# Optimization experiments

Hardware: AMD Instinct MI355X
Metric: run time of the kernel (lower is better)

The kernel has to match this reference:

```python
import jax, jax.numpy as jnp
import numpy as np

N, SPLIT, INPUT_DIM = 16384, 100, 128
NUM_HEADS, PER_DIM = 4, 64  # out_dim = 256
NEG_SLOPE = 0.2


def setup_inputs() -> dict:
    key = jax.random.key(0)
    kx, kw, kq = jax.random.split(key, 3)
    x = jax.random.normal(kx, (N, SPLIT * INPUT_DIM), dtype=jnp.float32)
    # glorot-uniform per-head projection weights [H, input_dim, per_dim]
    limit_w = float(np.sqrt(6.0 / (INPUT_DIM + PER_DIM)))
    W = jax.random.uniform(kw, (NUM_HEADS, INPUT_DIM, PER_DIM), dtype=jnp.float32,
                           minval=-limit_w, maxval=limit_w)
    # xavier-uniform query vectors (gain=1.414) for q_ of shape [per_dim, 1] -> stored [H, per_dim]
    limit_q = float(1.414 * np.sqrt(6.0 / (PER_DIM + 1)))
    q = jax.random.uniform(kq, (NUM_HEADS, PER_DIM), dtype=jnp.float32,
                           minval=-limit_q, maxval=limit_q)
    return {"x": x, "W": W, "q": q}


def reference(x, W, q):
    n = x.shape[0]
    xs = x.reshape(n, SPLIT, INPUT_DIM)                      # [n, s, i]
    h = jnp.einsum('nsi,hio->nhso', xs, W)                   # per-head projections
    score = jax.nn.leaky_relu(jnp.einsum('nhso,ho->nhs', h, q), NEG_SLOPE)
    att = jax.nn.softmax(score, axis=2)                      # softmax over split dim
    pooled = jnp.einsum('nhso,nhs->nho', h, att)             # weighted sum pooling
    return pooled.reshape(n, NUM_HEADS * PER_DIM)            # concat heads -> [n, out_dim]
```

## Files before the change

kernel.cpp:

```cpp
#include <hip/hip_runtime.h>
#include <stdint.h>

#define NROWS 16384
#define SPLITN 100
#define IDIM 128
#define NH 4
#define PD 64
#define ROWLEN (SPLITN * IDIM)
#define ODIM (NH * PD)

typedef float f32x4 __attribute__((ext_vector_type(4)));
typedef short s16x8 __attribute__((ext_vector_type(8)));
typedef unsigned short u16x8 __attribute__((ext_vector_type(8)));

__device__ __forceinline__ unsigned short f32_to_bf16(float f) {
  uint32_t u = __float_as_uint(f);
  u += 0x7FFFu + ((u >> 16) & 1u);
  return (unsigned short)(u >> 16);
}

#if __has_builtin(__builtin_amdgcn_exp2f)
__device__ __forceinline__ float fexp2(float x) { return __builtin_amdgcn_exp2f(x); }
#else
__device__ __forceinline__ float fexp2(float x) { return exp2f(x); }
#endif

template <int IMM>
__device__ __forceinline__ float swz_f(float v) {
  return __int_as_float(__builtin_amdgcn_ds_swizzle(__float_as_int(v), IMM));
}

__global__ void prep_wq(const float* __restrict__ W, const float* __restrict__ q,
                        float* __restrict__ wq) {
  int item = blockIdx.x * 256 + threadIdx.x;
  if (item >= NH * IDIM) return;
  int h = item >> 7, i = item & (IDIM - 1);
  const float* wrow = W + (size_t)(h * IDIM + i) * PD;
  const float* qh = q + h * PD;
  float s = 0.f;
#pragma unroll 8
  for (int o = 0; o < PD; ++o) s = __builtin_fmaf(wrow[o], qh[o], s);
  wq[item] = s;
}

__global__ void prep_wp(const float* __restrict__ W, unsigned short* __restrict__ Wp) {
  int flat = blockIdx.x * 256 + threadIdx.x;
  if (flat >= 64 * 512) return;
  int f = flat >> 9;
  int rem = flat & 511;
  int l = rem >> 3, j = rem & 7;
  int of = f & 3, kb = (f >> 2) & 3, h = f >> 4;
  int k = kb * 32 + (l >> 4) * 8 + j;
  int o = of * 16 + (l & 15);
  Wp[flat] = f32_to_bf16(W[(size_t)(h * IDIM + k) * PD + o]);
}

__global__ __launch_bounds__(256) void k1(const float* __restrict__ x,
                                          const float* __restrict__ wq,
                                          unsigned short* __restrict__ ybf) {
  const int lane = threadIdx.x & 63;
  const int g = lane >> 4;
  const int li = lane & 15;
  const int row = (blockIdx.x << 2) | (threadIdx.x >> 6);
  const float* xrow = x + (size_t)row * ROWLEN;

  float wqr[NH][8];
#pragma unroll
  for (int h = 0; h < NH; ++h) {
    f32x4 a = *(const f32x4*)(wq + h * IDIM + li * 8);
    f32x4 b = *(const f32x4*)(wq + h * IDIM + li * 8 + 4);
#pragma unroll
    for (int j = 0; j < 4; ++j) { wqr[h][j] = a[j]; wqr[h][4 + j] = b[j]; }
  }

  float y[NH][8];
  float m[NH], lsum[NH], mL[NH];
#pragma unroll
  for (int h = 0; h < NH; ++h) {
    m[h] = -INFINITY; mL[h] = -INFINITY; lsum[h] = 0.f;
#pragma unroll
    for (int j = 0; j < 8; ++j) y[h][j] = 0.f;
  }
  const float L2E = 1.44269504088896340736f;

  const float* pc = xrow + g * IDIM + li * 8;
  f32x4 xa = *(const f32x4*)pc;
  f32x4 xb = *(const f32x4*)(pc + 4);

  for (int it = 0; it < 25; ++it) {
    f32x4 na = {}, nb = {};
    const float* pn = pc + 4 * IDIM;
    if (it < 24) { na = *(const f32x4*)pn; nb = *(const f32x4*)(pn + 4); }

    float xv[8];
#pragma unroll
    for (int j = 0; j < 4; ++j) { xv[j] = xa[j]; xv[4 + j] = xb[j]; }

    float part[NH];
#pragma unroll
    for (int h = 0; h < NH; ++h) {
      float p = xv[0] * wqr[h][0];
#pragma unroll
      for (int j = 1; j < 8; ++j) p = __builtin_fmaf(xv[j], wqr[h][j], p);
      part[h] = p;
    }
#pragma unroll
    for (int h = 0; h < NH; ++h) {
      part[h] += swz_f<0x041F>(part[h]);
      part[h] += swz_f<0x081F>(part[h]);
      part[h] += swz_f<0x101F>(part[h]);
      part[h] += swz_f<0x201F>(part[h]);
    }
#pragma unroll
    for (int h = 0; h < NH; ++h) {
      float sc = part[h];
      sc = sc > 0.f ? sc : 0.2f * sc;
      if (sc > m[h] + 8.0f) {
        float scale = fexp2(mL[h] - sc * L2E);
        lsum[h] *= scale;
#pragma unroll
        for (int j = 0; j < 8; ++j) y[h][j] *= scale;
        m[h] = sc; mL[h] = sc * L2E;
      }
      float w = fexp2(__builtin_fmaf(sc, L2E, -mL[h]));
      lsum[h] += w;
#pragma unroll
      for (int j = 0; j < 8; ++j) y[h][j] = __builtin_fmaf(w, xv[j], y[h][j]);
    }
    xa = na; xb = nb; pc = pn;
  }

#pragma unroll
  for (int st = 16; st <= 32; st <<= 1) {
#pragma unroll
    for (int h = 0; h < NH; ++h) {
      float mo = __shfl_xor(m[h], st, 64);
      float lo = __shfl_xor(lsum[h], st, 64);
      float mn = fmaxf(m[h], mo);
      float ea = fexp2((m[h] - mn) * L2E);
      float eb = fexp2((mo - mn) * L2E);
      lsum[h] = lsum[h] * ea + lo * eb;
#pragma unroll
      for (int j = 0; j < 8; ++j) {
        float yo = __shfl_xor(y[h][j], st, 64);
        y[h][j] = y[h][j] * ea + yo * eb;
      }
      m[h] = mn;
    }
  }

  float lg = lsum[0];
  float ys[8];
#pragma unroll
  for (int j = 0; j < 8; ++j) ys[j] = y[0][j];
#pragma unroll
  for (int h = 1; h < NH; ++h) {
    bool sel = (g == h);
    lg = sel ? lsum[h] : lg;
#pragma unroll
    for (int j = 0; j < 8; ++j) ys[j] = sel ? y[h][j] : ys[j];
  }
  float inv = 1.0f / lg;
  u16x8 pk;
#pragma unroll
  for (int j = 0; j < 8; ++j) pk[j] = f32_to_bf16(ys[j] * inv);
  *(u16x8*)(ybf + (size_t)row * 512 + g * 128 + li * 8) = pk;
}

__global__ __launch_bounds__(256) void k2(const unsigned short* ybf,
                                          const unsigned short* __restrict__ Wp,
                                          float* out) {
  const int h = threadIdx.x >> 6;
  const int l = threadIdx.x & 63;
  const int rowb = blockIdx.x * 32;

  s16x8 Bf[4][4];
#pragma unroll
  for (int kb = 0; kb < 4; ++kb)
#pragma unroll
    for (int of = 0; of < 4; ++of)
      Bf[kb][of] = *(const s16x8*)(Wp + (size_t)(((h * 4 + kb) * 4 + of) * 512 + l * 8));

  s16x8 Af[2][4];
#pragma unroll
  for (int mf = 0; mf < 2; ++mf)
#pragma unroll
    for (int kb = 0; kb < 4; ++kb) {
      int r = rowb + mf * 16 + (l & 15);
      Af[mf][kb] = *(const s16x8*)(ybf + (size_t)r * 512 + h * 128 + kb * 32 + (l >> 4) * 8);
    }

  f32x4 acc[2][4];
#pragma unroll
  for (int mf = 0; mf < 2; ++mf)
#pragma unroll
    for (int of = 0; of < 4; ++of) acc[mf][of] = (f32x4){0.f, 0.f, 0.f, 0.f};

#pragma unroll
  for (int kb = 0; kb < 4; ++kb)
#pragma unroll
    for (int mf = 0; mf < 2; ++mf)
#pragma unroll
      for (int of = 0; of < 4; ++of)
        acc[mf][of] = __builtin_amdgcn_mfma_f32_16x16x32_bf16(Af[mf][kb], Bf[kb][of],
                                                              acc[mf][of], 0, 0, 0);

#pragma unroll
  for (int mf = 0; mf < 2; ++mf)
#pragma unroll
    for (int of = 0; of < 4; ++of)
#pragma unroll
      for (int reg = 0; reg < 4; ++reg) {
        int r = rowb + mf * 16 + (l >> 4) * 4 + reg;
        int o = of * 16 + (l & 15);
        out[(size_t)r * ODIM + h * PD + o] = acc[mf][of][reg];
      }
}

extern "C" void kernel_launch(void* const* d_in, const int* in_sizes, int n_in,
                              void* d_out, int out_size, void* d_ws, size_t ws_size,
                              hipStream_t stream) {
  const float* x = (const float*)d_in[0];
  const float* W = (const float*)d_in[1];
  const float* q = (const float*)d_in[2];
  float* out = (float*)d_out;
  float* wq = (float*)d_ws;
  unsigned short* Wp = (unsigned short*)((char*)d_ws + 2048);

  const size_t YOFF = (size_t)1 << 20;
  const size_t YBYTES = (size_t)NROWS * 512 * sizeof(unsigned short);
  unsigned short* ybf = (ws_size >= YOFF + YBYTES)
                            ? (unsigned short*)((char*)d_ws + YOFF)
                            : (unsigned short*)d_out;

  prep_wq<<<2, 256, 0, stream>>>(W, q, wq);
  prep_wp<<<128, 256, 0, stream>>>(W, Wp);
  k1<<<NROWS / 4, 256, 0, stream>>>(x, wq, ybf);
  k2<<<NROWS / 32, 256, 0, stream>>>(ybf, Wp, out);
}
```

Baseline: 178.0 us.

## Split each row across a whole block, merge softmax partials in LDS

The main kernel now gives each row to a 256-thread block: 16 streams of 16 lanes each take interleaved segments, instead of one wavefront handling one row. Partial online-softmax states are merged across the four wavefronts through shared memory. The change also switches to nontemporal loads without software prefetch and fuses the two prep kernels into one launch. It raises parallelism and memory-level concurrency per row, at the cost of a block barrier, LDS traffic and 4x more blocks with short loops.

```diff
diff --git a/kernel.cpp b/kernel.cpp
--- a/kernel.cpp
+++ b/kernel.cpp
@@ -30,39 +30,44 @@
   return __int_as_float(__builtin_amdgcn_ds_swizzle(__float_as_int(v), IMM));
 }
 
-__global__ void prep_wq(const float* __restrict__ W, const float* __restrict__ q,
-                        float* __restrict__ wq) {
-  int item = blockIdx.x * 256 + threadIdx.x;
-  if (item >= NH * IDIM) return;
-  int h = item >> 7, i = item & (IDIM - 1);
-  const float* wrow = W + (size_t)(h * IDIM + i) * PD;
-  const float* qh = q + h * PD;
-  float s = 0.f;
+__global__ void prep(const float* __restrict__ W, const float* __restrict__ q,
+                     float* __restrict__ wq, unsigned short* __restrict__ Wp) {
+  if (blockIdx.x < 128) {
+    int flat = blockIdx.x * 256 + threadIdx.x;
+    int f = flat >> 9;
+    int rem = flat & 511;
+    int l = rem >> 3, j = rem & 7;
+    int of = f & 3, kb = (f >> 2) & 3, h = f >> 4;
+    int k = kb * 32 + (l >> 4) * 8 + j;
+    int o = of * 16 + (l & 15);
+    Wp[flat] = f32_to_bf16(W[(size_t)(h * IDIM + k) * PD + o]);
+  } else {
+    for (int item = threadIdx.x; item < NH * IDIM; item += 256) {
+      int h = item >> 7, i = item & (IDIM - 1);
+      const float* wrow = W + (size_t)(h * IDIM + i) * PD;
+      const float* qh = q + h * PD;
+      float s = 0.f;
 #pragma unroll 8
-  for (int o = 0; o < PD; ++o) s = __builtin_fmaf(wrow[o], qh[o], s);
-  wq[item] = s;
-}
-
-__global__ void prep_wp(const float* __restrict__ W, unsigned short* __restrict__ Wp) {
-  int flat = blockIdx.x * 256 + threadIdx.x;
-  if (flat >= 64 * 512) return;
-  int f = flat >> 9;
-  int rem = flat & 511;
-  int l = rem >> 3, j = rem & 7;
-  int of = f & 3, kb = (f >> 2) & 3, h = f >> 4;
-  int k = kb * 32 + (l >> 4) * 8 + j;
-  int o = of * 16 + (l & 15);
-  Wp[flat] = f32_to_bf16(W[(size_t)(h * IDIM + k) * PD + o]);
+      for (int o = 0; o < PD; ++o) s = __builtin_fmaf(wrow[o], qh[o], s);
+      wq[item] = s;
+    }
+  }
 }
 
 __global__ __launch_bounds__(256) void k1(const float* __restrict__ x,
                                           const float* __restrict__ wq,
                                           unsigned short* __restrict__ ybf) {
+  const int w = threadIdx.x >> 6;
   const int lane = threadIdx.x & 63;
   const int g = lane >> 4;
   const int li = lane & 15;
-  const int row = (blockIdx.x << 2) | (threadIdx.x >> 6);
-  const float* xrow = x + (size_t)row * ROWLEN;
+  const int strm = w * 4 + g;
+  const int row = blockIdx.x;
+  const float* p = x + (size_t)row * ROWLEN + strm * IDIM + li * 8;
+
+  __shared__ float mLb[4][NH];
+  __shared__ float lb[4][NH];
+  __shared__ float yb[4][NH][128];
 
   float wqr[NH][8];
 #pragma unroll
@@ -83,14 +88,11 @@
   }
   const float L2E = 1.44269504088896340736f;
 
-  const float* pc = xrow + g * IDIM + li * 8;
-  f32x4 xa = *(const f32x4*)pc;
-  f32x4 xb = *(const f32x4*)(pc + 4);
-
-  for (int it = 0; it < 25; ++it) {
-    f32x4 na = {}, nb = {};
-    const float* pn = pc + 4 * IDIM;
-    if (it < 24) { na = *(const f32x4*)pn; nb = *(const f32x4*)(pn + 4); }
+  const int niter = (w == 0) ? 7 : 6;
+  for (int t = 0; t < niter; ++t) {
+    f32x4 xa = __builtin_nontemporal_load((const f32x4*)p);
+    f32x4 xb = __builtin_nontemporal_load((const f32x4*)(p + 4));
+    p += 16 * IDIM;
 
     float xv[8];
 #pragma unroll
@@ -99,10 +101,10 @@
     float part[NH];
 #pragma unroll
     for (int h = 0; h < NH; ++h) {
-      float p = xv[0] * wqr[h][0];
-#pragma unroll
-      for (int j = 1; j < 8; ++j) p = __builtin_fmaf(xv[j], wqr[h][j], p);
-      part[h] = p;
+      float pp = xv[0] * wqr[h][0];
+#pragma unroll
+      for (int j = 1; j < 8; ++j) pp = __builtin_fmaf(xv[j], wqr[h][j], pp);
+      part[h] = pp;
     }
 #pragma unroll
     for (int h = 0; h < NH; ++h) {
@@ -122,12 +124,11 @@
         for (int j = 0; j < 8; ++j) y[h][j] *= scale;
         m[h] = sc; mL[h] = sc * L2E;
       }
-      float w = fexp2(__builtin_fmaf(sc, L2E, -mL[h]));
-      lsum[h] += w;
-#pragma unroll
-      for (int j = 0; j < 8; ++j) y[h][j] = __builtin_fmaf(w, xv[j], y[h][j]);
-    }
-    xa = na; xb = nb; pc = pn;
+      float wgt = fexp2(__builtin_fmaf(sc, L2E, -mL[h]));
+      lsum[h] += wgt;
+#pragma unroll
+      for (int j = 0; j < 8; ++j) y[h][j] = __builtin_fmaf(wgt, xv[j], y[h][j]);
+    }
   }
 
 #pragma unroll
@@ -149,22 +150,44 @@
     }
   }
 
-  float lg = lsum[0];
-  float ys[8];
-#pragma unroll
-  for (int j = 0; j < 8; ++j) ys[j] = y[0][j];
-#pragma unroll
-  for (int h = 1; h < NH; ++h) {
-    bool sel = (g == h);
-    lg = sel ? lsum[h] : lg;
-#pragma unroll
-    for (int j = 0; j < 8; ++j) ys[j] = sel ? y[h][j] : ys[j];
-  }
-  float inv = 1.0f / lg;
-  u16x8 pk;
-#pragma unroll
-  for (int j = 0; j < 8; ++j) pk[j] = f32_to_bf16(ys[j] * inv);
-  *(u16x8*)(ybf + (size_t)row * 512 + g * 128 + li * 8) = pk;
+  if (lane < 16) {
+#pragma unroll
+    for (int h = 0; h < NH; ++h) {
+      *(f32x4*)&yb[w][h][li * 8]     = (f32x4){y[h][0], y[h][1], y[h][2], y[h][3]};
+      *(f32x4*)&yb[w][h][li * 8 + 4] = (f32x4){y[h][4], y[h][5], y[h][6], y[h][7]};
+    }
+    if (lane == 0) {
+#pragma unroll
+      for (int h = 0; h < NH; ++h) { mLb[w][h] = m[h] * L2E; lb[w][h] = lsum[h]; }
+    }
+  }
+  __syncthreads();
+
+  if (lane < 16) {
+    const int h = w;
+    float mm = fmaxf(fmaxf(mLb[0][h], mLb[1][h]), fmaxf(mLb[2][h], mLb[3][h]));
+    float ls = 0.f;
+    float yj[8];
+#pragma unroll
+    for (int j = 0; j < 8; ++j) yj[j] = 0.f;
+#pragma unroll
+    for (int ww = 0; ww < 4; ++ww) {
+      float e = fexp2(mLb[ww][h] - mm);
+      ls = __builtin_fmaf(lb[ww][h], e, ls);
+      f32x4 ya = *(const f32x4*)&yb[ww][h][li * 8];
+      f32x4 yc = *(const f32x4*)&yb[ww][h][li * 8 + 4];
+#pragma unroll
+      for (int j = 0; j < 4; ++j) {
+        yj[j] = __builtin_fmaf(ya[j], e, yj[j]);
+        yj[4 + j] = __builtin_fmaf(yc[j], e, yj[4 + j]);
+      }
+    }
+    float inv = 1.0f / ls;
+    u16x8 pk;
+#pragma unroll
+    for (int j = 0; j < 8; ++j) pk[j] = f32_to_bf16(yj[j] * inv);
+    *(u16x8*)(ybf + (size_t)row * 512 + h * 128 + li * 8) = pk;
+  }
 }
 
 __global__ __launch_bounds__(256) void k2(const unsigned short* ybf,
@@ -233,8 +256,7 @@
                             ? (unsigned short*)((char*)d_ws + YOFF)
                             : (unsigned short*)d_out;
 
-  prep_wq<<<2, 256, 0, stream>>>(W, q, wq);
-  prep_wp<<<128, 256, 0, stream>>>(W, Wp);
-  k1<<<NROWS / 4, 256, 0, stream>>>(x, wq, ybf);
+  prep<<<129, 256, 0, stream>>>(W, q, wq, Wp);
+  k1<<<NROWS, 256, 0, stream>>>(x, wq, ybf);
   k2<<<NROWS / 32, 256, 0, stream>>>(ybf, Wp, out);
 }
```

Measured after the change: 207.3 us. 1.16x slower.
